# Optimization experiments

Hardware: AMD Instinct MI355X
Metric: run time of the kernel (lower is better)

The kernel has to match this reference:

```python
import jax, jax.numpy as jnp
import numpy as np

HIDDEN = 4096
N_HEADS = 32
HEAD_DIM = HIDDEN // N_HEADS
MAX_POS = 2048
ROPE_BASE = 10000.0


def _rope_tables(head_dim, max_pos):
    inv_freq = 1.0 / (ROPE_BASE ** (np.arange(0, head_dim, 2, dtype=np.float32) / head_dim))
    t = np.arange(max_pos, dtype=np.float32)
    freqs = np.einsum('i,j->ij', t, inv_freq)          # [max_pos, head_dim//2]
    emb = np.concatenate([freqs, freqs], axis=-1)       # [max_pos, head_dim]
    return jnp.asarray(np.cos(emb)), jnp.asarray(np.sin(emb))


def _rotate_half(x):
    x1, x2 = jnp.split(x, 2, axis=-1)
    return jnp.concatenate([-x2, x1], axis=-1)


def setup_inputs() -> dict:
    key = jax.random.key(0)
    ks = jax.random.split(key, 5)
    B, S = 1, 2048
    hidden_states = jax.random.normal(ks[0], (B, S, HIDDEN), dtype=jnp.float32)
    # additive causal mask (0 on/below diagonal, large negative above)
    causal = jnp.triu(jnp.full((S, S), -1e9, dtype=jnp.float32), k=1)
    attention_mask = causal[None, None, :, :]
    scale = 0.02
    wq = jax.random.normal(ks[1], (HIDDEN, HIDDEN), dtype=jnp.float32) * scale
    wk = jax.random.normal(ks[2], (HIDDEN, HIDDEN), dtype=jnp.float32) * scale
    wv = jax.random.normal(ks[3], (HIDDEN, HIDDEN), dtype=jnp.float32) * scale
    wo = jax.random.normal(ks[4], (HIDDEN, HIDDEN), dtype=jnp.float32) * scale
    position_ids = jnp.arange(S, dtype=jnp.int64 if jax.config.jax_enable_x64 else jnp.int32)[None, :]
    return {"hidden_states": hidden_states, "attention_mask": attention_mask,
            "wq": wq, "wk": wk, "wv": wv, "wo": wo, "position_ids": position_ids}


def reference(hidden_states, attention_mask, wq, wk, wv, wo, position_ids):
    B, S, H = hidden_states.shape
    cos_tab, sin_tab = _rope_tables(HEAD_DIM, MAX_POS)

    def shape_heads(x):  # [B,S,H] -> [B,nH,S,hd]
        return x.reshape(B, S, N_HEADS, HEAD_DIM).transpose(0, 2, 1, 3)

    # QKV projections (torch Linear: x @ W.T, no bias)
    q = shape_heads(hidden_states @ wq.T)
    k = shape_heads(hidden_states @ wk.T)
    v = shape_heads(hidden_states @ wv.T)

    # RoPE
    cos = cos_tab[position_ids][:, None, :, :]  # [B,1,S,hd]
    sin = sin_tab[position_ids][:, None, :, :]
    q = q * cos + _rotate_half(q) * sin
    k = k * cos + _rotate_half(k) * sin

    # scaled dot-product attention
    scale = 1.0 / jnp.sqrt(jnp.float32(HEAD_DIM))
    scores = jnp.einsum('bhqd,bhkd->bhqk', q, k) * scale
    scores = scores + attention_mask  # broadcast over heads
    scores = jnp.maximum(scores, jnp.finfo(scores.dtype).min)
    probs = jax.nn.softmax(scores, axis=-1)
    attn = jnp.einsum('bhqk,bhkd->bhqd', probs, v)

    # merge heads, output projection
    attn = attn.transpose(0, 2, 1, 3).reshape(B, S, H)
    return attn @ wo.T
```

## Files before the change

kernel.cpp:

```cpp
#include <hip/hip_runtime.h>

typedef __bf16 bf16x8 __attribute__((ext_vector_type(8)));
typedef float f32x4 __attribute__((ext_vector_type(4)));

__device__ __forceinline__ ushort f2bf(float f) {
  uint u = __builtin_bit_cast(uint, f);
  u = (u + 0x7fffu + ((u >> 16) & 1u)) >> 16;
  return (ushort)u;
}
__device__ __forceinline__ ushort f2bf_fast(float f) {
  uint u = __builtin_bit_cast(uint, f);
  return (ushort)((u + 0x8000u) >> 16);
}
__device__ __forceinline__ float bf2f(ushort h) {
  uint u = ((uint)h) << 16;
  return __builtin_bit_cast(float, u);
}
__device__ __forceinline__ float ex2(float x) {
  return __builtin_amdgcn_exp2f(x);
}

__device__ __forceinline__ void gload16(const ushort* g, ushort* l) {
  __builtin_amdgcn_global_load_lds(
      (const __attribute__((address_space(1))) unsigned int*)(const void*)g,
      (__attribute__((address_space(3))) unsigned int*)(void*)l, 16, 0, 0);
}

__global__ void cvt_f32_bf16_k(const float* __restrict__ in, ushort* __restrict__ out, int n4) {
  int i = blockIdx.x * blockDim.x + threadIdx.x;
  if (i >= n4) return;
  float4 v = reinterpret_cast<const float4*>(in)[i];
  ushort4 o;
  o.x = f2bf(v.x); o.y = f2bf(v.y); o.z = f2bf(v.z); o.w = f2bf(v.w);
  reinterpret_cast<ushort4*>(out)[i] = o;
}

__global__ void rope_tables_k(float* __restrict__ cosT, float* __restrict__ sinT) {
  int i = blockIdx.x * 256 + threadIdx.x;
  int p = i >> 6, j = i & 63;
  float inv = powf(10000.0f, -(float)j / 64.0f);
  float ang = (float)p * inv;
  cosT[i] = cosf(ang);
  sinT[i] = sinf(ang);
}

__global__ void rope_k(ushort* __restrict__ Q, ushort* __restrict__ K,
                       const float* __restrict__ cosT, const float* __restrict__ sinT,
                       const int* __restrict__ pos) {
  int idx = blockIdx.x * 256 + threadIdx.x;
  int s = idx >> 11;
  int rest = idx & 2047;
  int h = rest >> 6, d = rest & 63;
  int p = pos[s];
  float c = cosT[p * 64 + d], sn = sinT[p * 64 + d];
  size_t base = (size_t)s * 4096 + h * 128 + d;
  float q1 = bf2f(Q[base]), q2 = bf2f(Q[base + 64]);
  Q[base]      = f2bf(q1 * c - q2 * sn);
  Q[base + 64] = f2bf(q2 * c + q1 * sn);
  float k1 = bf2f(K[base]), k2 = bf2f(K[base + 64]);
  K[base]      = f2bf(k1 * c - k2 * sn);
  K[base + 64] = f2bf(k2 * c + k1 * sn);
}

template<typename TA, typename TW, int OMODE>
__global__ __launch_bounds__(256) void gemm_bt(const TA* __restrict__ A, const TW* __restrict__ W,
                                               void* __restrict__ Cout) {
  constexpr int K = 4096, N = 4096, NT = K / 64;
  constexpr bool BF = (sizeof(TA) == 2 && sizeof(TW) == 2);
  __shared__ ushort As[2][128 * 64];
  __shared__ ushort Ws[2][128 * 64];
  const int tid = threadIdx.x;
  const int w = tid >> 6, lane = tid & 63, g = lane >> 4, r = lane & 15;
  const int wr = w >> 1, wc = w & 1;
  const int id = blockIdx.x;
  const int xcd = id & 7, slot = id >> 3;
  const int nb = (xcd & 3) * 8 + (slot & 7);
  const int mb = (xcd >> 2) * 8 + (slot >> 3);
  const int m0 = mb * 128, n0 = nb * 128;

  auto stage = [&](int t, int b) {
    const int k0 = t * 64;
    if constexpr (BF) {
#pragma unroll
      for (int i = 0; i < 4; i++) {
        int r0 = (w * 4 + i) * 8;
        int row = r0 + (lane >> 3), c = lane & 7;
        int cs = (c ^ (row & 7)) * 8;
        gload16((const ushort*)A + (size_t)(m0 + row) * K + k0 + cs, &As[b][r0 * 64]);
        gload16((const ushort*)W + (size_t)(n0 + row) * K + k0 + cs, &Ws[b][r0 * 64]);
      }
    } else {
#pragma unroll
      for (int i = 0; i < 4; i++) {
        int li = tid + i * 256, row = li >> 3, c = li & 7;
        int cs = (c ^ (row & 7)) * 8;
        const float* srcA = (const float*)A + (size_t)(m0 + row) * K + k0 + cs;
        float4 a0 = *reinterpret_cast<const float4*>(srcA);
        float4 a1 = *reinterpret_cast<const float4*>(srcA + 4);
        ushort oa[8] = {f2bf(a0.x), f2bf(a0.y), f2bf(a0.z), f2bf(a0.w),
                        f2bf(a1.x), f2bf(a1.y), f2bf(a1.z), f2bf(a1.w)};
        *reinterpret_cast<uint4*>(&As[b][row * 64 + c * 8]) = *reinterpret_cast<uint4*>(oa);
        const float* srcW = (const float*)W + (size_t)(n0 + row) * K + k0 + cs;
        float4 w0 = *reinterpret_cast<const float4*>(srcW);
        float4 w1 = *reinterpret_cast<const float4*>(srcW + 4);
        ushort ow[8] = {f2bf(w0.x), f2bf(w0.y), f2bf(w0.z), f2bf(w0.w),
                        f2bf(w1.x), f2bf(w1.y), f2bf(w1.z), f2bf(w1.w)};
        *reinterpret_cast<uint4*>(&Ws[b][row * 64 + c * 8]) = *reinterpret_cast<uint4*>(ow);
      }
    }
  };

  f32x4 acc[4][4];
#pragma unroll
  for (int i = 0; i < 4; i++)
#pragma unroll
    for (int j = 0; j < 4; j++) acc[i][j] = f32x4{0.f, 0.f, 0.f, 0.f};

  stage(0, 0);
  __syncthreads();

#pragma unroll 1
  for (int t = 0; t < NT; ++t) {
    const int buf = t & 1;
    if (t + 1 < NT) stage(t + 1, buf ^ 1);
#pragma unroll
    for (int kk = 0; kk < 2; kk++) {
      bf16x8 af[4], bfr[4];
#pragma unroll
      for (int mi = 0; mi < 4; mi++) {
        int row = wr * 64 + mi * 16 + r;
        af[mi] = *reinterpret_cast<const bf16x8*>((const char*)&As[buf][0] + row * 128 + (((g + kk * 4) ^ (r & 7)) * 16));
      }
#pragma unroll
      for (int nj = 0; nj < 4; nj++) {
        int row = wc * 64 + nj * 16 + r;
        bfr[nj] = *reinterpret_cast<const bf16x8*>((const char*)&Ws[buf][0] + row * 128 + (((g + kk * 4) ^ (r & 7)) * 16));
      }
#pragma unroll
      for (int mi = 0; mi < 4; mi++)
#pragma unroll
        for (int nj = 0; nj < 4; nj++)
          acc[mi][nj] = __builtin_amdgcn_mfma_f32_16x16x32_bf16(af[mi], bfr[nj], acc[mi][nj], 0, 0, 0);
    }
    __syncthreads();
  }

  if constexpr (OMODE == 0) {
    float* C = (float*)Cout;
#pragma unroll
    for (int mi = 0; mi < 4; mi++)
#pragma unroll
      for (int nj = 0; nj < 4; nj++)
#pragma unroll
        for (int j = 0; j < 4; j++) {
          int row = m0 + wr * 64 + mi * 16 + g * 4 + j;
          int col = n0 + wc * 64 + nj * 16 + r;
          C[(size_t)row * N + col] = acc[mi][nj][j];
        }
  } else if constexpr (OMODE == 1) {
    ushort* C = (ushort*)Cout;
#pragma unroll
    for (int mi = 0; mi < 4; mi++)
#pragma unroll
      for (int nj = 0; nj < 4; nj++)
#pragma unroll
        for (int j = 0; j < 4; j++) {
          int row = m0 + wr * 64 + mi * 16 + g * 4 + j;
          int col = n0 + wc * 64 + nj * 16 + r;
          C[(size_t)row * N + col] = f2bf(acc[mi][nj][j]);
        }
  } else {
    ushort* C = (ushort*)Cout;
#pragma unroll
    for (int mi = 0; mi < 4; mi++)
#pragma unroll
      for (int nj = 0; nj < 4; nj++) {
        int col = n0 + wc * 64 + nj * 16 + r;
        int row0 = m0 + wr * 64 + mi * 16 + g * 4;
        ushort4 v;
        v.x = f2bf(acc[mi][nj][0]); v.y = f2bf(acc[mi][nj][1]);
        v.z = f2bf(acc[mi][nj][2]); v.w = f2bf(acc[mi][nj][3]);
        *reinterpret_cast<ushort4*>(C + (size_t)col * 2048 + row0) = v;
      }
  }
}

__global__ __launch_bounds__(256) void attn_fwd(const ushort* __restrict__ Q, const ushort* __restrict__ K,
                                                const ushort* __restrict__ Vt, ushort* __restrict__ O) {
  constexpr int S = 2048, HD = 4096;
  constexpr float SC2 = 0.12753102f;
  constexpr float THR = 90.50967f;
  __shared__ ushort Ks[64 * 128];
  __shared__ ushort Vs[128 * 64];
  __shared__ ushort Ps[4][16 * 64];
  const int id = blockIdx.x;
  const int xcd = id & 7, rest = id >> 3;
  const int h = xcd * 4 + (rest & 3);
  const int qtile = 31 - (rest >> 2);
  const int qbase = qtile * 64;
  const int nt = qtile + 1;
  const int tid = threadIdx.x;
  const int w = tid >> 6, lane = tid & 63, g = lane >> 4, r = lane & 15;
  const int kRow = lane >> 4, kC = lane & 15;
  const int vRow = lane >> 3, vC = lane & 7;

  auto stage = [&](int t) {
    const int kv0 = t * 64;
#pragma unroll
    for (int i = 0; i < 4; i++) {
      int kr0 = (w * 4 + i) * 4, krow = kr0 + kRow;
      gload16(K + (size_t)(kv0 + krow) * HD + h * 128 + (kC ^ (krow & 7)) * 8, &Ks[kr0 * 128]);
      int vr0 = (w * 4 + i) * 8, vrow = vr0 + vRow;
      gload16(Vt + (size_t)(h * 128 + vrow) * S + kv0 + (vC ^ (vrow & 7)) * 8, &Vs[vr0 * 64]);
    }
  };

  bf16x8 qf[4];
  {
    const int qrow = qbase + w * 16 + r;
#pragma unroll
    for (int dc = 0; dc < 4; dc++)
      qf[dc] = *reinterpret_cast<const bf16x8*>(Q + (size_t)qrow * HD + h * 128 + dc * 32 + g * 8);
  }

  f32x4 o[8];
#pragma unroll
  for (int i = 0; i < 8; i++) o[i] = f32x4{0.f, 0.f, 0.f, 0.f};
  float m[4] = {-3e38f, -3e38f, -3e38f, -3e38f};
  float l[4] = {0.f, 0.f, 0.f, 0.f};

  stage(0);

#pragma unroll 1
  for (int t = 0; t < nt; ++t) {
    const int kv0 = t * 64;
    asm volatile("s_waitcnt vmcnt(0)" ::: "memory");
    __builtin_amdgcn_sched_barrier(0);
    __builtin_amdgcn_s_barrier();
    __builtin_amdgcn_sched_barrier(0);

    f32x4 sc[4];
    __builtin_amdgcn_s_setprio(1);
#pragma unroll
    for (int c = 0; c < 4; c++) {
      f32x4 tacc = f32x4{0.f, 0.f, 0.f, 0.f};
      const int krow = c * 16 + r;
      const char* kb = (const char*)&Ks[0] + krow * 256;
#pragma unroll
      for (int dc = 0; dc < 4; dc++) {
        bf16x8 kf = *reinterpret_cast<const bf16x8*>(kb + ((dc * 64 + g * 16) ^ ((krow & 7) << 4)));
        tacc = __builtin_amdgcn_mfma_f32_16x16x32_bf16(qf[dc], kf, tacc, 0, 0, 0);
      }
      sc[c] = tacc;
    }
    __builtin_amdgcn_s_setprio(0);

    if (t == nt - 1) {
#pragma unroll
      for (int c = 0; c < 4; c++) {
        int kvg = kv0 + c * 16 + r;
#pragma unroll
        for (int j = 0; j < 4; j++) {
          int qg = qbase + w * 16 + g * 4 + j;
          if (kvg > qg) sc[c][j] = -3e38f;
        }
      }
    }

    float pl[4];
#pragma unroll
    for (int j = 0; j < 4; j++)
      pl[j] = fmaxf(fmaxf(sc[0][j], sc[1][j]), fmaxf(sc[2][j], sc[3][j]));
    bool ok = (pl[0] - m[0] <= THR) && (pl[1] - m[1] <= THR) &&
              (pl[2] - m[2] <= THR) && (pl[3] - m[3] <= THR);
    if (!__all(ok)) {
      float pm[4] = {pl[0], pl[1], pl[2], pl[3]};
#pragma unroll
      for (int st = 1; st < 16; st <<= 1) {
        float t0 = __shfl_xor(pm[0], st);
        float t1 = __shfl_xor(pm[1], st);
        float t2 = __shfl_xor(pm[2], st);
        float t3 = __shfl_xor(pm[3], st);
        pm[0] = fmaxf(pm[0], t0); pm[1] = fmaxf(pm[1], t1);
        pm[2] = fmaxf(pm[2], t2); pm[3] = fmaxf(pm[3], t3);
      }
#pragma unroll
      for (int j = 0; j < 4; j++) {
        float mn = fmaxf(m[j], pm[j]);
        float alpha = ex2((m[j] - mn) * SC2);
        m[j] = mn;
        l[j] *= alpha;
#pragma unroll
        for (int dc = 0; dc < 8; dc++) o[dc][j] *= alpha;
      }
    }

    char* pb = (char*)&Ps[w][0];
#pragma unroll
    for (int j = 0; j < 4; j++) {
      float mb = m[j] * SC2;
      float p0 = ex2(__builtin_fmaf(sc[0][j], SC2, -mb));
      float p1 = ex2(__builtin_fmaf(sc[1][j], SC2, -mb));
      float p2 = ex2(__builtin_fmaf(sc[2][j], SC2, -mb));
      float p3 = ex2(__builtin_fmaf(sc[3][j], SC2, -mb));
      l[j] += (p0 + p1) + (p2 + p3);
      int ql = g * 4 + j;
      char* pr = pb + (size_t)ql * 128;
      uint sw = (ql & 7) << 4;
      *reinterpret_cast<ushort*>(pr + ((0 * 32 + r * 2) ^ sw)) = f2bf_fast(p0);
      *reinterpret_cast<ushort*>(pr + ((1 * 32 + r * 2) ^ sw)) = f2bf_fast(p1);
      *reinterpret_cast<ushort*>(pr + ((2 * 32 + r * 2) ^ sw)) = f2bf_fast(p2);
      *reinterpret_cast<ushort*>(pr + ((3 * 32 + r * 2) ^ sw)) = f2bf_fast(p3);
    }

    __builtin_amdgcn_s_setprio(1);
#pragma unroll
    for (int c2 = 0; c2 < 2; c2++) {
      bf16x8 pf = *reinterpret_cast<const bf16x8*>(pb + (size_t)r * 128 + ((c2 * 64 + g * 16) ^ ((r & 7) << 4)));
#pragma unroll
      for (int dc = 0; dc < 8; dc++) {
        const int vrow = dc * 16 + r;
        bf16x8 vf = *reinterpret_cast<const bf16x8*>((const char*)&Vs[0] + vrow * 128 + ((c2 * 64 + g * 16) ^ ((vrow & 7) << 4)));
        o[dc] = __builtin_amdgcn_mfma_f32_16x16x32_bf16(pf, vf, o[dc], 0, 0, 0);
      }
    }
    __builtin_amdgcn_s_setprio(0);

    __syncthreads();
    if (t + 1 < nt) stage(t + 1);
  }

#pragma unroll
  for (int st = 1; st < 16; st <<= 1) {
    float t0 = __shfl_xor(l[0], st);
    float t1 = __shfl_xor(l[1], st);
    float t2 = __shfl_xor(l[2], st);
    float t3 = __shfl_xor(l[3], st);
    l[0] += t0; l[1] += t1; l[2] += t2; l[3] += t3;
  }
  float rl[4];
#pragma unroll
  for (int j = 0; j < 4; j++) rl[j] = __builtin_amdgcn_rcpf(l[j]);
#pragma unroll
  for (int dc = 0; dc < 8; dc++)
#pragma unroll
    for (int j = 0; j < 4; j++) {
      float v = o[dc][j] * rl[j];
      O[(size_t)(qbase + w * 16 + g * 4 + j) * HD + h * 128 + dc * 16 + r] = f2bf(v);
    }
}

extern "C" void kernel_launch(void* const* d_in, const int* in_sizes, int n_in,
                              void* d_out, int out_size, void* d_ws, size_t ws_size,
                              hipStream_t stream) {
  const float* X  = (const float*)d_in[0];
  const float* Wq = (const float*)d_in[2];
  const float* Wk = (const float*)d_in[3];
  const float* Wv = (const float*)d_in[4];
  const float* Wo = (const float*)d_in[5];
  const int* pos  = (const int*)d_in[6];
  float* out = (float*)d_out;
  char* ws = (char*)d_ws;
  const size_t MB = 1024ull * 1024ull;

  float*  tabC = (float*)(ws + 0);
  float*  tabS = (float*)(ws + 512 * 1024);
  ushort* Qb   = (ushort*)(ws + 1 * MB);
  ushort* Kb   = (ushort*)(ws + 17 * MB);
  ushort* Vt   = (ushort*)(ws + 33 * MB);
  ushort* Ab   = (ushort*)(ws + 49 * MB);
  ushort* Xb   = (ushort*)(ws + 65 * MB);
  ushort* Wb   = (ushort*)(ws + 81 * MB);
  const bool fast = ws_size >= 113 * MB;

  rope_tables_k<<<512, 256, 0, stream>>>(tabC, tabS);

  if (fast) {
    cvt_f32_bf16_k<<<8192, 256, 0, stream>>>(X, Xb, 2097152);
    cvt_f32_bf16_k<<<16384, 256, 0, stream>>>(Wq, Wb, 4194304);
    gemm_bt<ushort, ushort, 1><<<512, 256, 0, stream>>>(Xb, Wb, Qb);
    cvt_f32_bf16_k<<<16384, 256, 0, stream>>>(Wk, Wb, 4194304);
    gemm_bt<ushort, ushort, 1><<<512, 256, 0, stream>>>(Xb, Wb, Kb);
    cvt_f32_bf16_k<<<16384, 256, 0, stream>>>(Wv, Wb, 4194304);
    gemm_bt<ushort, ushort, 2><<<512, 256, 0, stream>>>(Xb, Wb, Vt);
    rope_k<<<16384, 256, 0, stream>>>(Qb, Kb, tabC, tabS, pos);
    attn_fwd<<<1024, 256, 0, stream>>>(Qb, Kb, Vt, Ab);
    cvt_f32_bf16_k<<<16384, 256, 0, stream>>>(Wo, Wb, 4194304);
    gemm_bt<ushort, ushort, 0><<<512, 256, 0, stream>>>(Ab, Wb, out);
  } else {
    gemm_bt<float, float, 1><<<512, 256, 0, stream>>>(X, Wq, Qb);
    gemm_bt<float, float, 1><<<512, 256, 0, stream>>>(X, Wk, Kb);
    gemm_bt<float, float, 2><<<512, 256, 0, stream>>>(X, Wv, Vt);
    rope_k<<<16384, 256, 0, stream>>>(Qb, Kb, tabC, tabS, pos);
    attn_fwd<<<1024, 256, 0, stream>>>(Qb, Kb, Vt, Ab);
    gemm_bt<ushort, float, 0><<<512, 256, 0, stream>>>(Ab, Wo, out);
  }
}
```

Before: 447.3 us.

## Fuse fp32 weight conversion into GEMM with register-staged prefetch

Drops the four separate fp32-to-bf16 weight conversion kernels and has the GEMM read fp32 weights directly, converting them while staging into shared memory. The weight tile for the next iteration is loaded into registers before the MFMA loop and converted and written to LDS after it, so global load latency overlaps compute. This removes a write and re-read of 32MB of bf16 weights per projection, in exchange for twice the global bytes per weight tile inside the GEMM and higher register pressure from the eight float4 staging registers.

```diff
diff --git a/kernel.cpp b/kernel.cpp
--- a/kernel.cpp
+++ b/kernel.cpp
@@ -66,7 +66,6 @@
 __global__ __launch_bounds__(256) void gemm_bt(const TA* __restrict__ A, const TW* __restrict__ W,
                                                void* __restrict__ Cout) {
   constexpr int K = 4096, N = 4096, NT = K / 64;
-  constexpr bool BF = (sizeof(TA) == 2 && sizeof(TW) == 2);
   __shared__ ushort As[2][128 * 64];
   __shared__ ushort Ws[2][128 * 64];
   const int tid = threadIdx.x;
@@ -78,51 +77,87 @@
   const int mb = (xcd >> 2) * 8 + (slot >> 3);
   const int m0 = mb * 128, n0 = nb * 128;
 
-  auto stage = [&](int t, int b) {
+  auto stageA = [&](int t, int b) {
     const int k0 = t * 64;
-    if constexpr (BF) {
+    if constexpr (sizeof(TA) == 2) {
 #pragma unroll
       for (int i = 0; i < 4; i++) {
         int r0 = (w * 4 + i) * 8;
         int row = r0 + (lane >> 3), c = lane & 7;
         int cs = (c ^ (row & 7)) * 8;
         gload16((const ushort*)A + (size_t)(m0 + row) * K + k0 + cs, &As[b][r0 * 64]);
-        gload16((const ushort*)W + (size_t)(n0 + row) * K + k0 + cs, &Ws[b][r0 * 64]);
       }
     } else {
 #pragma unroll
       for (int i = 0; i < 4; i++) {
         int li = tid + i * 256, row = li >> 3, c = li & 7;
         int cs = (c ^ (row & 7)) * 8;
-        const float* srcA = (const float*)A + (size_t)(m0 + row) * K + k0 + cs;
-        float4 a0 = *reinterpret_cast<const float4*>(srcA);
-        float4 a1 = *reinterpret_cast<const float4*>(srcA + 4);
+        const float* src = (const float*)A + (size_t)(m0 + row) * K + k0 + cs;
+        float4 a0 = *reinterpret_cast<const float4*>(src);
+        float4 a1 = *reinterpret_cast<const float4*>(src + 4);
         ushort oa[8] = {f2bf(a0.x), f2bf(a0.y), f2bf(a0.z), f2bf(a0.w),
                         f2bf(a1.x), f2bf(a1.y), f2bf(a1.z), f2bf(a1.w)};
         *reinterpret_cast<uint4*>(&As[b][row * 64 + c * 8]) = *reinterpret_cast<uint4*>(oa);
-        const float* srcW = (const float*)W + (size_t)(n0 + row) * K + k0 + cs;
-        float4 w0 = *reinterpret_cast<const float4*>(srcW);
-        float4 w1 = *reinterpret_cast<const float4*>(srcW + 4);
-        ushort ow[8] = {f2bf(w0.x), f2bf(w0.y), f2bf(w0.z), f2bf(w0.w),
-                        f2bf(w1.x), f2bf(w1.y), f2bf(w1.z), f2bf(w1.w)};
-        *reinterpret_cast<uint4*>(&Ws[b][row * 64 + c * 8]) = *reinterpret_cast<uint4*>(ow);
       }
     }
   };
 
+  float4 wreg[8];
+  auto stageW_bf = [&](int t, int b) {
+    const int k0 = t * 64;
+#pragma unroll
+    for (int i = 0; i < 4; i++) {
+      int r0 = (w * 4 + i) * 8;
+      int row = r0 + (lane >> 3), c = lane & 7;
+      int cs = (c ^ (row & 7)) * 8;
+      gload16((const ushort*)W + (size_t)(n0 + row) * K + k0 + cs, &Ws[b][r0 * 64]);
+    }
+  };
+  auto issueW = [&](int t) {
+    const int k0 = t * 64;
+#pragma unroll
+    for (int i = 0; i < 4; i++) {
+      int li = tid + i * 256, row = li >> 3, c = li & 7;
+      int cs = (c ^ (row & 7)) * 8;
+      const float* src = (const float*)W + (size_t)(n0 + row) * K + k0 + cs;
+      wreg[2 * i]     = *reinterpret_cast<const float4*>(src);
+      wreg[2 * i + 1] = *reinterpret_cast<const float4*>(src + 4);
+    }
+  };
+  auto commitW = [&](int b) {
+#pragma unroll
+    for (int i = 0; i < 4; i++) {
+      int li = tid + i * 256, row = li >> 3, c = li & 7;
+      float4 w0 = wreg[2 * i], w1 = wreg[2 * i + 1];
+      ushort ow[8] = {f2bf(w0.x), f2bf(w0.y), f2bf(w0.z), f2bf(w0.w),
+                      f2bf(w1.x), f2bf(w1.y), f2bf(w1.z), f2bf(w1.w)};
+      *reinterpret_cast<uint4*>(&Ws[b][row * 64 + c * 8]) = *reinterpret_cast<uint4*>(ow);
+    }
+  };
+
   f32x4 acc[4][4];
 #pragma unroll
   for (int i = 0; i < 4; i++)
 #pragma unroll
     for (int j = 0; j < 4; j++) acc[i][j] = f32x4{0.f, 0.f, 0.f, 0.f};
 
-  stage(0, 0);
+  stageA(0, 0);
+  if constexpr (sizeof(TW) == 2) stageW_bf(0, 0);
+  else { issueW(0); commitW(0); }
   __syncthreads();
 
 #pragma unroll 1
   for (int t = 0; t < NT; ++t) {
     const int buf = t & 1;
-    if (t + 1 < NT) stage(t + 1, buf ^ 1);
+    if (t + 1 < NT) {
+      if constexpr (sizeof(TW) == 2) {
+        stageA(t + 1, buf ^ 1);
+        stageW_bf(t + 1, buf ^ 1);
+      } else {
+        issueW(t + 1);
+        stageA(t + 1, buf ^ 1);
+      }
+    }
 #pragma unroll
     for (int kk = 0; kk < 2; kk++) {
       bf16x8 af[4], bfr[4];
@@ -141,6 +176,9 @@
 #pragma unroll
         for (int nj = 0; nj < 4; nj++)
           acc[mi][nj] = __builtin_amdgcn_mfma_f32_16x16x32_bf16(af[mi], bfr[nj], acc[mi][nj], 0, 0, 0);
+    }
+    if constexpr (sizeof(TW) != 2) {
+      if (t + 1 < NT) commitW(buf ^ 1);
     }
     __syncthreads();
   }
@@ -370,23 +408,18 @@
   ushort* Vt   = (ushort*)(ws + 33 * MB);
   ushort* Ab   = (ushort*)(ws + 49 * MB);
   ushort* Xb   = (ushort*)(ws + 65 * MB);
-  ushort* Wb   = (ushort*)(ws + 81 * MB);
-  const bool fast = ws_size >= 113 * MB;
+  const bool fast = ws_size >= 82 * MB;
 
   rope_tables_k<<<512, 256, 0, stream>>>(tabC, tabS);
 
   if (fast) {
     cvt_f32_bf16_k<<<8192, 256, 0, stream>>>(X, Xb, 2097152);
-    cvt_f32_bf16_k<<<16384, 256, 0, stream>>>(Wq, Wb, 4194304);
-    gemm_bt<ushort, ushort, 1><<<512, 256, 0, stream>>>(Xb, Wb, Qb);
-    cvt_f32_bf16_k<<<16384, 256, 0, stream>>>(Wk, Wb, 4194304);
-    gemm_bt<ushort, ushort, 1><<<512, 256, 0, stream>>>(Xb, Wb, Kb);
-    cvt_f32_bf16_k<<<16384, 256, 0, stream>>>(Wv, Wb, 4194304);
-    gemm_bt<ushort, ushort, 2><<<512, 256, 0, stream>>>(Xb, Wb, Vt);
+    gemm_bt<ushort, float, 1><<<512, 256, 0, stream>>>(Xb, Wq, Qb);
+    gemm_bt<ushort, float, 1><<<512, 256, 0, stream>>>(Xb, Wk, Kb);
+    gemm_bt<ushort, float, 2><<<512, 256, 0, stream>>>(Xb, Wv, Vt);
     rope_k<<<16384, 256, 0, stream>>>(Qb, Kb, tabC, tabS, pos);
     attn_fwd<<<1024, 256, 0, stream>>>(Qb, Kb, Vt, Ab);
-    cvt_f32_bf16_k<<<16384, 256, 0, stream>>>(Wo, Wb, 4194304);
-    gemm_bt<ushort, ushort, 0><<<512, 256, 0, stream>>>(Ab, Wb, out);
+    gemm_bt<ushort, float, 0><<<512, 256, 0, stream>>>(Ab, Wo, out);
   } else {
     gemm_bt<float, float, 1><<<512, 256, 0, stream>>>(X, Wq, Qb);
     gemm_bt<float, float, 1><<<512, 256, 0, stream>>>(X, Wk, Kb);
```

Measured after the change: 528.7 us. 18.2% more time.

## Fuse next weight's fp32-to-bf16 conversion into the preceding GEMM loop

Applied to the files above, without the earlier changes.

Each projection GEMM now converts the next weight matrix from fp32 to bf16 inside its k-loop, writing into a second ping-pong bf16 weight buffer. This removes three standalone conversion launches and hides the conversion traffic behind MFMA work. Each GEMM gains extra global loads and stores plus register pressure. The fused path only runs when the workspace is at least 145 MB, otherwise the old paths are used.

```diff
diff --git a/kernel.cpp b/kernel.cpp
--- a/kernel.cpp
+++ b/kernel.cpp
@@ -64,7 +64,9 @@
 
 template<typename TA, typename TW, int OMODE>
 __global__ __launch_bounds__(256) void gemm_bt(const TA* __restrict__ A, const TW* __restrict__ W,
-                                               void* __restrict__ Cout) {
+                                               void* __restrict__ Cout,
+                                               const float* __restrict__ Wn,
+                                               ushort* __restrict__ Wnb) {
   constexpr int K = 4096, N = 4096, NT = K / 64;
   constexpr bool BF = (sizeof(TA) == 2 && sizeof(TW) == 2);
   __shared__ ushort As[2][128 * 64];
@@ -122,6 +124,12 @@
 #pragma unroll 1
   for (int t = 0; t < NT; ++t) {
     const int buf = t & 1;
+    float2 cv;
+    size_t cbase = 0;
+    if (Wn) {
+      cbase = ((size_t)t * 131072 + (size_t)id * 256 + tid) * 2;
+      cv = *reinterpret_cast<const float2*>(Wn + cbase);
+    }
     if (t + 1 < NT) stage(t + 1, buf ^ 1);
 #pragma unroll
     for (int kk = 0; kk < 2; kk++) {
@@ -141,6 +149,12 @@
 #pragma unroll
         for (int nj = 0; nj < 4; nj++)
           acc[mi][nj] = __builtin_amdgcn_mfma_f32_16x16x32_bf16(af[mi], bfr[nj], acc[mi][nj], 0, 0, 0);
+    }
+    if (Wn) {
+      ushort2 o;
+      o.x = f2bf(cv.x);
+      o.y = f2bf(cv.y);
+      *reinterpret_cast<ushort2*>(Wnb + cbase) = o;
     }
     __syncthreads();
   }
@@ -370,29 +384,39 @@
   ushort* Vt   = (ushort*)(ws + 33 * MB);
   ushort* Ab   = (ushort*)(ws + 49 * MB);
   ushort* Xb   = (ushort*)(ws + 65 * MB);
-  ushort* Wb   = (ushort*)(ws + 81 * MB);
-  const bool fast = ws_size >= 113 * MB;
+  ushort* Wb0  = (ushort*)(ws + 81 * MB);
+  ushort* Wb1  = (ushort*)(ws + 113 * MB);
 
   rope_tables_k<<<512, 256, 0, stream>>>(tabC, tabS);
 
-  if (fast) {
+  if (ws_size >= 145 * MB) {
+    cvt_f32_bf16_k<<<8192, 256, 0, stream>>>(X, Xb, 2097152);
+    cvt_f32_bf16_k<<<16384, 256, 0, stream>>>(Wq, Wb0, 4194304);
+    gemm_bt<ushort, ushort, 1><<<512, 256, 0, stream>>>(Xb, Wb0, Qb, Wk, Wb1);
+    gemm_bt<ushort, ushort, 1><<<512, 256, 0, stream>>>(Xb, Wb1, Kb, Wv, Wb0);
+    gemm_bt<ushort, ushort, 2><<<512, 256, 0, stream>>>(Xb, Wb0, Vt, Wo, Wb1);
+    rope_k<<<16384, 256, 0, stream>>>(Qb, Kb, tabC, tabS, pos);
+    attn_fwd<<<1024, 256, 0, stream>>>(Qb, Kb, Vt, Ab);
+    gemm_bt<ushort, ushort, 0><<<512, 256, 0, stream>>>(Ab, Wb1, out, nullptr, nullptr);
+  } else if (ws_size >= 113 * MB) {
+    ushort* Wb = Wb0;
     cvt_f32_bf16_k<<<8192, 256, 0, stream>>>(X, Xb, 2097152);
     cvt_f32_bf16_k<<<16384, 256, 0, stream>>>(Wq, Wb, 4194304);
-    gemm_bt<ushort, ushort, 1><<<512, 256, 0, stream>>>(Xb, Wb, Qb);
+    gemm_bt<ushort, ushort, 1><<<512, 256, 0, stream>>>(Xb, Wb, Qb, nullptr, nullptr);
     cvt_f32_bf16_k<<<16384, 256, 0, stream>>>(Wk, Wb, 4194304);
-    gemm_bt<ushort, ushort, 1><<<512, 256, 0, stream>>>(Xb, Wb, Kb);
+    gemm_bt<ushort, ushort, 1><<<512, 256, 0, stream>>>(Xb, Wb, Kb, nullptr, nullptr);
     cvt_f32_bf16_k<<<16384, 256, 0, stream>>>(Wv, Wb, 4194304);
-    gemm_bt<ushort, ushort, 2><<<512, 256, 0, stream>>>(Xb, Wb, Vt);
+    gemm_bt<ushort, ushort, 2><<<512, 256, 0, stream>>>(Xb, Wb, Vt, nullptr, nullptr);
     rope_k<<<16384, 256, 0, stream>>>(Qb, Kb, tabC, tabS, pos);
     attn_fwd<<<1024, 256, 0, stream>>>(Qb, Kb, Vt, Ab);
     cvt_f32_bf16_k<<<16384, 256, 0, stream>>>(Wo, Wb, 4194304);
-    gemm_bt<ushort, ushort, 0><<<512, 256, 0, stream>>>(Ab, Wb, out);
+    gemm_bt<ushort, ushort, 0><<<512, 256, 0, stream>>>(Ab, Wb, out, nullptr, nullptr);
   } else {
-    gemm_bt<float, float, 1><<<512, 256, 0, stream>>>(X, Wq, Qb);
-    gemm_bt<float, float, 1><<<512, 256, 0, stream>>>(X, Wk, Kb);
-    gemm_bt<float, float, 2><<<512, 256, 0, stream>>>(X, Wv, Vt);
+    gemm_bt<float, float, 1><<<512, 256, 0, stream>>>(X, Wq, Qb, nullptr, nullptr);
+    gemm_bt<float, float, 1><<<512, 256, 0, stream>>>(X, Wk, Kb, nullptr, nullptr);
+    gemm_bt<float, float, 2><<<512, 256, 0, stream>>>(X, Wv, Vt, nullptr, nullptr);
     rope_k<<<16384, 256, 0, stream>>>(Qb, Kb, tabC, tabS, pos);
     attn_fwd<<<1024, 256, 0, stream>>>(Qb, Kb, Vt, Ab);
-    gemm_bt<ushort, float, 0><<<512, 256, 0, stream>>>(Ab, Wo, out);
-  }
-}
+    gemm_bt<ushort, float, 0><<<512, 256, 0, stream>>>(Ab, Wo, out, nullptr, nullptr);
+  }
+}
```

New measurement: 462.2 us. +3.3%, slower.

## Fuse Q, K and V projections into a single batched GEMM launch

Applied to the files above, without the earlier changes.

Converts all three QKV weight matrices to bf16 into separate workspace regions up front. It then runs one 1536-block GEMM in which each block picks its output (Q, K, or transposed V) by column-block index. This removes two kernel launches and the per-launch tail effects, and lets X tiles be shared across more concurrent blocks. In exchange it needs a larger workspace (177MB), and it falls back to the old path if that workspace is not available.

```diff
diff --git a/kernel.cpp b/kernel.cpp
--- a/kernel.cpp
+++ b/kernel.cpp
@@ -60,6 +60,100 @@
   float k1 = bf2f(K[base]), k2 = bf2f(K[base + 64]);
   K[base]      = f2bf(k1 * c - k2 * sn);
   K[base + 64] = f2bf(k2 * c + k1 * sn);
+}
+
+__global__ __launch_bounds__(256) void gemm_qkv(const ushort* __restrict__ A,
+                                                const ushort* __restrict__ W,
+                                                ushort* __restrict__ Qb,
+                                                ushort* __restrict__ Kb,
+                                                ushort* __restrict__ Vt) {
+  constexpr int K = 4096, NT = K / 64;
+  __shared__ ushort As[2][128 * 64];
+  __shared__ ushort Ws[2][128 * 64];
+  const int tid = threadIdx.x;
+  const int w = tid >> 6, lane = tid & 63, g = lane >> 4, r = lane & 15;
+  const int wr = w >> 1, wc = w & 1;
+  const int id = blockIdx.x;
+  const int xcd = id & 7, slot = id >> 3;
+  const int sm = slot / 24, sn = slot % 24;
+  const int nb = (xcd & 3) * 24 + sn;
+  const int mb = (xcd >> 2) * 8 + sm;
+  const int m0 = mb * 128, n0 = nb * 128;
+
+  auto stage = [&](int t, int b) {
+    const int k0 = t * 64;
+#pragma unroll
+    for (int i = 0; i < 4; i++) {
+      int r0 = (w * 4 + i) * 8;
+      int row = r0 + (lane >> 3), c = lane & 7;
+      int cs = (c ^ (row & 7)) * 8;
+      gload16(A + (size_t)(m0 + row) * K + k0 + cs, &As[b][r0 * 64]);
+      gload16(W + (size_t)(n0 + row) * K + k0 + cs, &Ws[b][r0 * 64]);
+    }
+  };
+
+  f32x4 acc[4][4];
+#pragma unroll
+  for (int i = 0; i < 4; i++)
+#pragma unroll
+    for (int j = 0; j < 4; j++) acc[i][j] = f32x4{0.f, 0.f, 0.f, 0.f};
+
+  stage(0, 0);
+  __syncthreads();
+
+#pragma unroll 1
+  for (int t = 0; t < NT; ++t) {
+    const int buf = t & 1;
+    if (t + 1 < NT) stage(t + 1, buf ^ 1);
+#pragma unroll
+    for (int kk = 0; kk < 2; kk++) {
+      bf16x8 af[4], bfr[4];
+#pragma unroll
+      for (int mi = 0; mi < 4; mi++) {
+        int row = wr * 64 + mi * 16 + r;
+        af[mi] = *reinterpret_cast<const bf16x8*>((const char*)&As[buf][0] + row * 128 + (((g + kk * 4) ^ (r & 7)) * 16));
+      }
+#pragma unroll
+      for (int nj = 0; nj < 4; nj++) {
+        int row = wc * 64 + nj * 16 + r;
+        bfr[nj] = *reinterpret_cast<const bf16x8*>((const char*)&Ws[buf][0] + row * 128 + (((g + kk * 4) ^ (r & 7)) * 16));
+      }
+#pragma unroll
+      for (int mi = 0; mi < 4; mi++)
+#pragma unroll
+        for (int nj = 0; nj < 4; nj++)
+          acc[mi][nj] = __builtin_amdgcn_mfma_f32_16x16x32_bf16(af[mi], bfr[nj], acc[mi][nj], 0, 0, 0);
+    }
+    __syncthreads();
+  }
+
+  if (nb < 64) {
+    ushort* C = (nb < 32) ? Qb : Kb;
+    const int cb = (nb & 31) * 128;
+#pragma unroll
+    for (int mi = 0; mi < 4; mi++)
+#pragma unroll
+      for (int nj = 0; nj < 4; nj++)
+#pragma unroll
+        for (int j = 0; j < 4; j++) {
+          int row = m0 + wr * 64 + mi * 16 + g * 4 + j;
+          int col = cb + wc * 64 + nj * 16 + r;
+          C[(size_t)row * 4096 + col] = f2bf(acc[mi][nj][j]);
+        }
+  } else {
+    const int vb = (nb - 64) * 128;
+#pragma unroll
+    for (int mi = 0; mi < 4; mi++)
+#pragma unroll
+      for (int nj = 0; nj < 4; nj++) {
+        int col = vb + wc * 64 + nj * 16 + r;
+        int row0 = m0 + wr * 64 + mi * 16 + g * 4;
+        ushort4 v;
+        v.x = f2bf(acc[mi][nj][0]); v.y = f2bf(acc[mi][nj][1]);
+        v.z = f2bf(acc[mi][nj][2]); v.w = f2bf(acc[mi][nj][3]);
+        *reinterpret_cast<ushort4*>(Vt + (size_t)col * 2048 + row0) = v;
+      }
+  }
 }
 
 template<typename TA, typename TW, int OMODE>
@@ -371,11 +465,20 @@
   ushort* Ab   = (ushort*)(ws + 49 * MB);
   ushort* Xb   = (ushort*)(ws + 65 * MB);
   ushort* Wb   = (ushort*)(ws + 81 * MB);
-  const bool fast = ws_size >= 113 * MB;
 
   rope_tables_k<<<512, 256, 0, stream>>>(tabC, tabS);
 
-  if (fast) {
+  if (ws_size >= 177 * MB) {
+    cvt_f32_bf16_k<<<8192, 256, 0, stream>>>(X, Xb, 2097152);
+    cvt_f32_bf16_k<<<16384, 256, 0, stream>>>(Wq, Wb, 4194304);
+    cvt_f32_bf16_k<<<16384, 256, 0, stream>>>(Wk, Wb + 16777216, 4194304);
+    cvt_f32_bf16_k<<<16384, 256, 0, stream>>>(Wv, Wb + 33554432, 4194304);
+    gemm_qkv<<<1536, 256, 0, stream>>>(Xb, Wb, Qb, Kb, Vt);
+    rope_k<<<16384, 256, 0, stream>>>(Qb, Kb, tabC, tabS, pos);
+    attn_fwd<<<1024, 256, 0, stream>>>(Qb, Kb, Vt, Ab);
+    cvt_f32_bf16_k<<<16384, 256, 0, stream>>>(Wo, Wb, 4194304);
+    gemm_bt<ushort, ushort, 0><<<512, 256, 0, stream>>>(Ab, Wb, out);
+  } else if (ws_size >= 113 * MB) {
     cvt_f32_bf16_k<<<8192, 256, 0, stream>>>(X, Xb, 2097152);
     cvt_f32_bf16_k<<<16384, 256, 0, stream>>>(Wq, Wb, 4194304);
     gemm_bt<ushort, ushort, 1><<<512, 256, 0, stream>>>(Xb, Wb, Qb);
```

Result: slower. 472.0 us (+5.5%).
